# Optimization experiments

Measured on AMD Instinct MI355X. Metric: run time of the kernel, lower is better.

## Reference

```python
import jax, jax.numpy as jnp
import numpy as np
import math

D_MODEL = 1024
D_HIDDEN = 64
H = 16
B = 2
N = 2048


def softmax_one(x, axis=-1):
    # exp(x - max) / (1 + sum(exp(x - max))) -- matches the torch code exactly
    m = jnp.max(x, axis=axis, keepdims=True)
    e = jnp.exp(x - m)
    return e / (1.0 + jnp.sum(e, axis=axis, keepdims=True))


def setup_inputs() -> dict:
    key = jax.random.key(0)
    ks = jax.random.split(key, 8)
    queries = jax.random.normal(ks[0], (B, N, D_MODEL), dtype=jnp.float32)
    keys = jax.random.normal(ks[1], (B, N, D_MODEL), dtype=jnp.float32)
    values = jax.random.normal(ks[2], (B, N, D_MODEL), dtype=jnp.float32)
    std = 0.02
    Wq = std * jax.random.normal(ks[3], (H * D_HIDDEN, D_MODEL), dtype=jnp.float32)
    Wk = std * jax.random.normal(ks[4], (H * D_HIDDEN, D_MODEL), dtype=jnp.float32)
    Wv = std * jax.random.normal(ks[5], (H * D_HIDDEN, D_MODEL), dtype=jnp.float32)
    Wo = std * jax.random.normal(ks[6], (D_MODEL, H * D_HIDDEN), dtype=jnp.float32)
    bq = jnp.zeros((H * D_HIDDEN,), jnp.float32)
    bk = jnp.zeros((H * D_HIDDEN,), jnp.float32)
    bv = jnp.zeros((H * D_HIDDEN,), jnp.float32)
    bo = jnp.zeros((D_MODEL,), jnp.float32)
    return {"queries": queries, "keys": keys, "values": values,
            "Wq": Wq, "bq": bq, "Wk": Wk, "bk": bk,
            "Wv": Wv, "bv": bv, "Wo": Wo, "bo": bo}


def reference(queries, keys, values, Wq, bq, Wk, bk, Wv, bv, Wo, bo):
    b_s, nq, _ = queries.shape
    nk = keys.shape[1]
    # projections: (b, n, h*dh) -> (b, h, n, dh)
    q = (queries @ Wq.T + bq).reshape(b_s, nq, H, D_HIDDEN).transpose(0, 2, 1, 3)
    k = (keys @ Wk.T + bk).reshape(b_s, nk, H, D_HIDDEN).transpose(0, 2, 1, 3)
    v = (values @ Wv.T + bv).reshape(b_s, nk, H, D_HIDDEN).transpose(0, 2, 1, 3)
    scale = 1.0 / math.sqrt(D_HIDDEN)
    scores = jnp.einsum('bhqd,bhkd->bhqk', q, k) * scale  # (b, h, nq, nk)
    attn = softmax_one(scores, axis=-1)  # dropout disabled (eval)
    out = jnp.einsum('bhqk,bhkd->bhqd', attn, v)  # (b, h, nq, dh)
    out = out.transpose(0, 2, 1, 3).reshape(b_s, nq, H * D_HIDDEN)
    out = out @ Wo.T + bo
    present = jnp.stack((k, v))  # (2, b, h, nk, dh)
    return (out, present)
```

## Files before the change

kernel.cpp:

```cpp
#include <hip/hip_runtime.h>
#include <math.h>

#define D_MODEL 1024
#define DH 64
#define NH 16
#define BS 2
#define SEQ 2048
#define MTOT (BS*SEQ)

typedef _Float16 f16x8 __attribute__((ext_vector_type(8)));
typedef _Float16 f16x4 __attribute__((ext_vector_type(4)));
typedef float f32x4 __attribute__((ext_vector_type(4)));

__global__ __launch_bounds__(256) void convert3_kernel(
    const float* __restrict__ s0, const float* __restrict__ s1, const float* __restrict__ s2,
    _Float16* __restrict__ d0, _Float16* __restrict__ d1, _Float16* __restrict__ d2, int n)
{
    const float* s = (blockIdx.y == 0) ? s0 : (blockIdx.y == 1) ? s1 : s2;
    _Float16* d    = (blockIdx.y == 0) ? d0 : (blockIdx.y == 1) ? d1 : d2;
    int i = (blockIdx.x * 256 + threadIdx.x) * 8;
    if (i < n) {
        float4 a = *(const float4*)(s + i);
        float4 b = *(const float4*)(s + i + 4);
        f16x8 o;
        o[0] = (_Float16)a.x; o[1] = (_Float16)a.y; o[2] = (_Float16)a.z; o[3] = (_Float16)a.w;
        o[4] = (_Float16)b.x; o[5] = (_Float16)b.y; o[6] = (_Float16)b.z; o[7] = (_Float16)b.w;
        *(f16x8*)(d + i) = o;
    }
}

__global__ __launch_bounds__(256) void qkv_proj_kernel(
    const _Float16* __restrict__ Xq, const _Float16* __restrict__ Xk, const _Float16* __restrict__ Xv,
    const _Float16* __restrict__ Wq, const _Float16* __restrict__ Wk, const _Float16* __restrict__ Wv,
    const float* __restrict__ bq, const float* __restrict__ bk, const float* __restrict__ bv,
    _Float16* __restrict__ qh, _Float16* __restrict__ kh, _Float16* __restrict__ vt,
    float* __restrict__ outp)
{
    __shared__ __align__(16) _Float16 ldsA[128][40];
    __shared__ __align__(16) _Float16 ldsB[128][40];

    const int jb = blockIdx.x >> 5;
    const int ib = blockIdx.x & 31;
    const int id = jb >> 3;
    const int col0 = (jb & 7) << 7;
    const int row0 = ib << 7;

    const _Float16* X  = (id == 0) ? Xq : (id == 1) ? Xk : Xv;
    const _Float16* W  = (id == 0) ? Wq : (id == 1) ? Wk : Wv;
    const float* bias  = (id == 0) ? bq : (id == 1) ? bk : bv;

    const int tid = threadIdx.x;
    const int w = tid >> 6, lane = tid & 63;
    const int quad = lane >> 4, l16 = lane & 15;
    const int wm = (w >> 1) << 6, wn = (w & 1) << 6;

    const f32x4 zero = {0.f, 0.f, 0.f, 0.f};
    f32x4 acc[4][4];
#pragma unroll
    for (int i = 0; i < 4; i++)
#pragma unroll
        for (int j = 0; j < 4; j++) acc[i][j] = zero;

    for (int k0 = 0; k0 < D_MODEL; k0 += 32) {
        __syncthreads();
#pragma unroll
        for (int i = 0; i < 2; i++) {
            int c = tid + 256 * i;
            int r = c >> 2, c8 = (c & 3) << 3;
            *(f16x8*)&ldsA[r][c8] = *(const f16x8*)(X + (size_t)(row0 + r) * D_MODEL + k0 + c8);
            *(f16x8*)&ldsB[r][c8] = *(const f16x8*)(W + (size_t)(col0 + r) * D_MODEL + k0 + c8);
        }
        __syncthreads();
        f16x8 af[4], bfr[4];
#pragma unroll
        for (int mi = 0; mi < 4; mi++) af[mi]  = *(const f16x8*)&ldsA[wm + mi*16 + l16][quad*8];
#pragma unroll
        for (int ni = 0; ni < 4; ni++) bfr[ni] = *(const f16x8*)&ldsB[wn + ni*16 + l16][quad*8];
#pragma unroll
        for (int mi = 0; mi < 4; mi++)
#pragma unroll
            for (int ni = 0; ni < 4; ni++)
                acc[mi][ni] = __builtin_amdgcn_mfma_f32_16x16x32_f16(af[mi], bfr[ni], acc[mi][ni], 0, 0, 0);
    }

    const size_t OUT0 = (size_t)MTOT * D_MODEL;
    const size_t PRES = (size_t)BS * NH * SEQ * DH;
#pragma unroll
    for (int ni = 0; ni < 4; ni++) {
        int gn = col0 + wn + ni * 16 + l16;
        float bias_v = bias[gn];
        int h = gn >> 6, d = gn & 63;
#pragma unroll
        for (int mi = 0; mi < 4; mi++) {
#pragma unroll
            for (int r = 0; r < 4; r++) {
                int gm = row0 + wm + mi * 16 + quad * 4 + r;
                float val = acc[mi][ni][r] + bias_v;
                int b = gm >> 11, n = gm & 2047;
                size_t bh = (size_t)(b * NH + h);
                size_t idx = (bh * SEQ + n) * DH + d;
                if (id == 0) {
                    qh[idx] = (_Float16)val;
                } else if (id == 1) {
                    outp[OUT0 + idx] = val;
                    kh[idx] = (_Float16)val;
                } else {
                    outp[OUT0 + PRES + idx] = val;
                    vt[(bh * DH + d) * SEQ + n] = (_Float16)val;
                }
            }
        }
    }
}

__global__ __launch_bounds__(256) void attn_kernel(
    const _Float16* __restrict__ qh, const _Float16* __restrict__ kh,
    const _Float16* __restrict__ vt, _Float16* __restrict__ aout)
{
    __shared__ __align__(16) _Float16 Kt[64][72];
    __shared__ __align__(16) _Float16 Vt[64][72];

    const int bh = blockIdx.x & 31;
    const int qt = blockIdx.x >> 5;
    const int b = bh >> 4, h = bh & 15;
    const int tid = threadIdx.x;
    const int w = tid >> 6, lane = tid & 63;
    const int quad = lane >> 4, l16 = lane & 15;
    const int qr0 = qt * 64 + w * 16;

    const _Float16* Qb = qh + (size_t)bh * SEQ * DH;
    const _Float16* Kb = kh + (size_t)bh * SEQ * DH;
    const _Float16* Vb = vt + (size_t)bh * DH * SEQ;

    const float QSCALE = 0.125f * 1.44269504f;
    f16x8 aq[2];
#pragma unroll
    for (int ks = 0; ks < 2; ks++) {
        f16x8 t = *(const f16x8*)(Qb + (size_t)(qr0 + l16) * DH + ks * 32 + quad * 8);
#pragma unroll
        for (int j = 0; j < 8; j++) t[j] = (_Float16)((float)t[j] * QSCALE);
        aq[ks] = t;
    }

    float m2 = -INFINITY, lsum = 0.f;
    const f32x4 zero = {0.f, 0.f, 0.f, 0.f};
    f32x4 accO[4];
#pragma unroll
    for (int db = 0; db < 4; db++) accO[db] = zero;

    for (int kc = 0; kc < SEQ; kc += 64) {
        __syncthreads();
#pragma unroll
        for (int i = 0; i < 2; i++) {
            int c = tid + 256 * i;
            int r = c >> 3, c8 = (c & 7) << 3;
            *(f16x8*)&Kt[r][c8] = *(const f16x8*)(Kb + (size_t)(kc + r) * DH + c8);
            *(f16x8*)&Vt[r][c8] = *(const f16x8*)(Vb + (size_t)r * SEQ + kc + c8);
        }
        __syncthreads();

        f32x4 sT[4];
#pragma unroll
        for (int nb = 0; nb < 4; nb++) sT[nb] = zero;
#pragma unroll
        for (int ks = 0; ks < 2; ks++)
#pragma unroll
            for (int nb = 0; nb < 4; nb++) {
                f16x8 kf = *(const f16x8*)&Kt[nb*16 + l16][ks*32 + quad*8];
                sT[nb] = __builtin_amdgcn_mfma_f32_16x16x32_f16(kf, aq[ks], sT[nb], 0, 0, 0);
            }

        float smax = -INFINITY;
#pragma unroll
        for (int nb = 0; nb < 4; nb++)
#pragma unroll
            for (int r = 0; r < 4; r++) smax = fmaxf(smax, sT[nb][r]);
        smax = fmaxf(smax, __shfl_xor(smax, 16));
        smax = fmaxf(smax, __shfl_xor(smax, 32));
        float m2new = fmaxf(m2, smax);
        float alpha = __builtin_amdgcn_exp2f(m2 - m2new);

        float tsum = 0.f;
#pragma unroll
        for (int nb = 0; nb < 4; nb++)
#pragma unroll
            for (int r = 0; r < 4; r++) {
                float e = __builtin_amdgcn_exp2f(sT[nb][r] - m2new);
                sT[nb][r] = e;
                tsum += e;
            }
        tsum += __shfl_xor(tsum, 16);
        tsum += __shfl_xor(tsum, 32);
        lsum = lsum * alpha + tsum;
        m2 = m2new;

#pragma unroll
        for (int db = 0; db < 4; db++)
#pragma unroll
            for (int r = 0; r < 4; r++) accO[db][r] *= alpha;

        f16x4 pf[4];
#pragma unroll
        for (int nb = 0; nb < 4; nb++)
#pragma unroll
            for (int r = 0; r < 4; r++) pf[nb][r] = (_Float16)sT[nb][r];

#pragma unroll
        for (int db = 0; db < 4; db++)
#pragma unroll
            for (int nb = 0; nb < 4; nb++) {
                f16x4 vf = *(const f16x4*)&Vt[db*16 + l16][nb*16 + quad*4];
                accO[db] = __builtin_amdgcn_mfma_f32_16x16x16f16(vf, pf[nb], accO[db], 0, 0, 0);
            }
    }

    const float inv = 1.f / (1.f + lsum);
    const int q = qr0 + l16;
    _Float16* orow = aout + ((size_t)b * SEQ + q) * D_MODEL + h * DH + quad * 4;
#pragma unroll
    for (int db = 0; db < 4; db++) {
        f16x4 o;
#pragma unroll
        for (int r = 0; r < 4; r++) o[r] = (_Float16)(accO[db][r] * inv);
        *(f16x4*)(orow + db * 16) = o;
    }
}

__global__ __launch_bounds__(256) void out_proj_kernel(
    const _Float16* __restrict__ aout, const _Float16* __restrict__ Wo,
    const float* __restrict__ bo, float* __restrict__ outp)
{
    __shared__ __align__(16) _Float16 ldsA[128][40];
    __shared__ __align__(16) _Float16 ldsB[128][40];

    const int jb = blockIdx.x >> 5;
    const int ib = blockIdx.x & 31;
    const int col0 = jb << 7, row0 = ib << 7;
    const int tid = threadIdx.x;
    const int w = tid >> 6, lane = tid & 63;
    const int quad = lane >> 4, l16 = lane & 15;
    const int wm = (w >> 1) << 6, wn = (w & 1) << 6;

    const f32x4 zero = {0.f, 0.f, 0.f, 0.f};
    f32x4 acc[4][4];
#pragma unroll
    for (int i = 0; i < 4; i++)
#pragma unroll
        for (int j = 0; j < 4; j++) acc[i][j] = zero;

    for (int k0 = 0; k0 < D_MODEL; k0 += 32) {
        __syncthreads();
#pragma unroll
        for (int i = 0; i < 2; i++) {
            int c = tid + 256 * i;
            int r = c >> 2, c8 = (c & 3) << 3;
            *(f16x8*)&ldsA[r][c8] = *(const f16x8*)(aout + (size_t)(row0 + r) * D_MODEL + k0 + c8);
            *(f16x8*)&ldsB[r][c8] = *(const f16x8*)(Wo   + (size_t)(col0 + r) * D_MODEL + k0 + c8);
        }
        __syncthreads();
        f16x8 af[4], bfr[4];
#pragma unroll
        for (int mi = 0; mi < 4; mi++) af[mi]  = *(const f16x8*)&ldsA[wm + mi*16 + l16][quad*8];
#pragma unroll
        for (int ni = 0; ni < 4; ni++) bfr[ni] = *(const f16x8*)&ldsB[wn + ni*16 + l16][quad*8];
#pragma unroll
        for (int mi = 0; mi < 4; mi++)
#pragma unroll
            for (int ni = 0; ni < 4; ni++)
                acc[mi][ni] = __builtin_amdgcn_mfma_f32_16x16x32_f16(af[mi], bfr[ni], acc[mi][ni], 0, 0, 0);
    }

#pragma unroll
    for (int ni = 0; ni < 4; ni++) {
        int gn = col0 + wn + ni * 16 + l16;
        float bias_v = bo[gn];
#pragma unroll
        for (int mi = 0; mi < 4; mi++)
#pragma unroll
            for (int r = 0; r < 4; r++) {
                int gm = row0 + wm + mi * 16 + quad * 4 + r;
                outp[(size_t)gm * D_MODEL + gn] = acc[mi][ni][r] + bias_v;
            }
    }
}

extern "C" void kernel_launch(void* const* d_in, const int* in_sizes, int n_in,
                              void* d_out, int out_size, void* d_ws, size_t ws_size,
                              hipStream_t stream)
{
    const float* queries = (const float*)d_in[0];
    const float* keys    = (const float*)d_in[1];
    const float* values  = (const float*)d_in[2];
    const float* Wq = (const float*)d_in[3];
    const float* bq = (const float*)d_in[4];
    const float* Wk = (const float*)d_in[5];
    const float* bk = (const float*)d_in[6];
    const float* Wv = (const float*)d_in[7];
    const float* bv = (const float*)d_in[8];
    const float* Wo = (const float*)d_in[9];
    const float* bo = (const float*)d_in[10];
    float* outp = (float*)d_out;

    const size_t NELT = (size_t)BS * NH * SEQ * DH;
    const size_t XN   = (size_t)MTOT * D_MODEL;
    const size_t WN   = (size_t)D_MODEL * D_MODEL;
    _Float16* qh   = (_Float16*)d_ws;
    _Float16* kh   = qh + NELT;
    _Float16* vt   = kh + NELT;
    _Float16* aout = vt + NELT;
    _Float16* Xfq  = aout + NELT;
    _Float16* Xfk  = Xfq + XN;
    _Float16* Xfv  = Xfk + XN;
    _Float16* Wfq  = Xfv + XN;
    _Float16* Wfk  = Wfq + WN;
    _Float16* Wfv  = Wfk + WN;
    _Float16* Wfo  = Wfv + WN;

    convert3_kernel<<<dim3((int)(XN/2048), 3), dim3(256), 0, stream>>>(
        queries, keys, values, Xfq, Xfk, Xfv, (int)XN);
    convert3_kernel<<<dim3((int)(WN/2048), 3), dim3(256), 0, stream>>>(
        Wq, Wk, Wv, Wfq, Wfk, Wfv, (int)WN);
    convert3_kernel<<<dim3((int)(WN/2048), 1), dim3(256), 0, stream>>>(
        Wo, Wo, Wo, Wfo, Wfo, Wfo, (int)WN);

    qkv_proj_kernel<<<dim3(768), dim3(256), 0, stream>>>(
        Xfq, Xfk, Xfv, Wfq, Wfk, Wfv, bq, bk, bv, qh, kh, vt, outp);
    attn_kernel<<<dim3(1024), dim3(256), 0, stream>>>(qh, kh, vt, aout);
    out_proj_kernel<<<dim3(256), dim3(256), 0, stream>>>(aout, Wfo, bo, outp);
}
```

Baseline: 278.9 us.

## Merge convert launches, use direct global-to-LDS loads, double-buffer attention K/V

```diff
diff --git a/kernel.cpp b/kernel.cpp
--- a/kernel.cpp
+++ b/kernel.cpp
@@ -11,13 +11,33 @@
 typedef _Float16 f16x8 __attribute__((ext_vector_type(8)));
 typedef _Float16 f16x4 __attribute__((ext_vector_type(4)));
 typedef float f32x4 __attribute__((ext_vector_type(4)));
-
-__global__ __launch_bounds__(256) void convert3_kernel(
+typedef unsigned int u32;
+
+__device__ __forceinline__ void load_lds16(const void* g, void* l) {
+    __builtin_amdgcn_global_load_lds(
+        (const __attribute__((address_space(1))) u32*)g,
+        (__attribute__((address_space(3))) u32*)l, 16, 0, 0);
+}
+
+__global__ __launch_bounds__(256) void convert_all_kernel(
     const float* __restrict__ s0, const float* __restrict__ s1, const float* __restrict__ s2,
-    _Float16* __restrict__ d0, _Float16* __restrict__ d1, _Float16* __restrict__ d2, int n)
-{
-    const float* s = (blockIdx.y == 0) ? s0 : (blockIdx.y == 1) ? s1 : s2;
-    _Float16* d    = (blockIdx.y == 0) ? d0 : (blockIdx.y == 1) ? d1 : d2;
+    const float* __restrict__ s3, const float* __restrict__ s4, const float* __restrict__ s5,
+    const float* __restrict__ s6,
+    _Float16* __restrict__ d0, _Float16* __restrict__ d1, _Float16* __restrict__ d2,
+    _Float16* __restrict__ d3, _Float16* __restrict__ d4, _Float16* __restrict__ d5,
+    _Float16* __restrict__ d6, int nX, int nW)
+{
+    int y = blockIdx.y;
+    const float* s; _Float16* d; int n;
+    switch (y) {
+        case 0: s = s0; d = d0; n = nX; break;
+        case 1: s = s1; d = d1; n = nX; break;
+        case 2: s = s2; d = d2; n = nX; break;
+        case 3: s = s3; d = d3; n = nW; break;
+        case 4: s = s4; d = d4; n = nW; break;
+        case 5: s = s5; d = d5; n = nW; break;
+        default: s = s6; d = d6; n = nW; break;
+    }
     int i = (blockIdx.x * 256 + threadIdx.x) * 8;
     if (i < n) {
         float4 a = *(const float4*)(s + i);
@@ -36,8 +56,8 @@
     _Float16* __restrict__ qh, _Float16* __restrict__ kh, _Float16* __restrict__ vt,
     float* __restrict__ outp)
 {
-    __shared__ __align__(16) _Float16 ldsA[128][40];
-    __shared__ __align__(16) _Float16 ldsB[128][40];
+    __shared__ __align__(16) _Float16 ldsA[128][32];
+    __shared__ __align__(16) _Float16 ldsB[128][32];
 
     const int jb = blockIdx.x >> 5;
     const int ib = blockIdx.x & 31;
@@ -54,6 +74,9 @@
     const int quad = lane >> 4, l16 = lane & 15;
     const int wm = (w >> 1) << 6, wn = (w & 1) << 6;
 
+    const int srow = w * 16 + (lane >> 2);
+    const int scol = (lane & 3) << 3;
+
     const f32x4 zero = {0.f, 0.f, 0.f, 0.f};
     f32x4 acc[4][4];
 #pragma unroll
@@ -65,10 +88,9 @@
         __syncthreads();
 #pragma unroll
         for (int i = 0; i < 2; i++) {
-            int c = tid + 256 * i;
-            int r = c >> 2, c8 = (c & 3) << 3;
-            *(f16x8*)&ldsA[r][c8] = *(const f16x8*)(X + (size_t)(row0 + r) * D_MODEL + k0 + c8);
-            *(f16x8*)&ldsB[r][c8] = *(const f16x8*)(W + (size_t)(col0 + r) * D_MODEL + k0 + c8);
+            int r = i * 64 + srow;
+            load_lds16(X + (size_t)(row0 + r) * D_MODEL + k0 + scol, &ldsA[i * 64 + w * 16][0]);
+            load_lds16(W + (size_t)(col0 + r) * D_MODEL + k0 + scol, &ldsB[i * 64 + w * 16][0]);
         }
         __syncthreads();
         f16x8 af[4], bfr[4];
@@ -117,8 +139,8 @@
     const _Float16* __restrict__ qh, const _Float16* __restrict__ kh,
     const _Float16* __restrict__ vt, _Float16* __restrict__ aout)
 {
-    __shared__ __align__(16) _Float16 Kt[64][72];
-    __shared__ __align__(16) _Float16 Vt[64][72];
+    __shared__ __align__(16) _Float16 Kt[2][64][76];
+    __shared__ __align__(16) _Float16 Vt[2][64][76];
 
     const int bh = blockIdx.x & 31;
     const int qt = blockIdx.x >> 5;
@@ -142,22 +164,36 @@
         aq[ks] = t;
     }
 
+    const int sr0 = tid >> 3, sc = (tid & 7) << 3;
+    const int sr1 = sr0 + 32;
+
+    {
+        *(f16x8*)&Kt[0][sr0][sc] = *(const f16x8*)(Kb + (size_t)sr0 * DH + sc);
+        *(f16x8*)&Kt[0][sr1][sc] = *(const f16x8*)(Kb + (size_t)sr1 * DH + sc);
+        *(f16x8*)&Vt[0][sr0][sc] = *(const f16x8*)(Vb + (size_t)sr0 * SEQ + sc);
+        *(f16x8*)&Vt[0][sr1][sc] = *(const f16x8*)(Vb + (size_t)sr1 * SEQ + sc);
+    }
+    __syncthreads();
+
     float m2 = -INFINITY, lsum = 0.f;
     const f32x4 zero = {0.f, 0.f, 0.f, 0.f};
     f32x4 accO[4];
 #pragma unroll
     for (int db = 0; db < 4; db++) accO[db] = zero;
 
-    for (int kc = 0; kc < SEQ; kc += 64) {
-        __syncthreads();
-#pragma unroll
-        for (int i = 0; i < 2; i++) {
-            int c = tid + 256 * i;
-            int r = c >> 3, c8 = (c & 7) << 3;
-            *(f16x8*)&Kt[r][c8] = *(const f16x8*)(Kb + (size_t)(kc + r) * DH + c8);
-            *(f16x8*)&Vt[r][c8] = *(const f16x8*)(Vb + (size_t)r * SEQ + kc + c8);
-        }
-        __syncthreads();
+    for (int t = 0; t < SEQ / 64; t++) {
+        const int cur = t & 1;
+        const int kc = t * 64;
+
+        f16x8 kr0, kr1, vr0, vr1;
+        if (t + 1 < SEQ / 64) {
+            const _Float16* kp = Kb + (size_t)(kc + 64) * DH;
+            const _Float16* vp = Vb + kc + 64;
+            kr0 = *(const f16x8*)(kp + (size_t)sr0 * DH + sc);
+            kr1 = *(const f16x8*)(kp + (size_t)sr1 * DH + sc);
+            vr0 = *(const f16x8*)(vp + (size_t)sr0 * SEQ + sc);
+            vr1 = *(const f16x8*)(vp + (size_t)sr1 * SEQ + sc);
+        }
 
         f32x4 sT[4];
 #pragma unroll
@@ -166,7 +202,7 @@
         for (int ks = 0; ks < 2; ks++)
 #pragma unroll
             for (int nb = 0; nb < 4; nb++) {
-                f16x8 kf = *(const f16x8*)&Kt[nb*16 + l16][ks*32 + quad*8];
+                f16x8 kf = *(const f16x8*)&Kt[cur][nb*16 + l16][ks*32 + quad*8];
                 sT[nb] = __builtin_amdgcn_mfma_f32_16x16x32_f16(kf, aq[ks], sT[nb], 0, 0, 0);
             }
 
@@ -209,9 +245,17 @@
         for (int db = 0; db < 4; db++)
 #pragma unroll
             for (int nb = 0; nb < 4; nb++) {
-                f16x4 vf = *(const f16x4*)&Vt[db*16 + l16][nb*16 + quad*4];
+                f16x4 vf = *(const f16x4*)&Vt[cur][db*16 + l16][nb*16 + quad*4];
                 accO[db] = __builtin_amdgcn_mfma_f32_16x16x16f16(vf, pf[nb], accO[db], 0, 0, 0);
             }
+
+        if (t + 1 < SEQ / 64) {
+            *(f16x8*)&Kt[cur ^ 1][sr0][sc] = kr0;
+            *(f16x8*)&Kt[cur ^ 1][sr1][sc] = kr1;
+            *(f16x8*)&Vt[cur ^ 1][sr0][sc] = vr0;
+            *(f16x8*)&Vt[cur ^ 1][sr1][sc] = vr1;
+        }
+        __syncthreads();
     }
 
     const float inv = 1.f / (1.f + lsum);
@@ -230,8 +274,8 @@
     const _Float16* __restrict__ aout, const _Float16* __restrict__ Wo,
     const float* __restrict__ bo, float* __restrict__ outp)
 {
-    __shared__ __align__(16) _Float16 ldsA[128][40];
-    __shared__ __align__(16) _Float16 ldsB[128][40];
+    __shared__ __align__(16) _Float16 ldsA[128][32];
+    __shared__ __align__(16) _Float16 ldsB[128][32];
 
     const int jb = blockIdx.x >> 5;
     const int ib = blockIdx.x & 31;
@@ -241,6 +285,9 @@
     const int quad = lane >> 4, l16 = lane & 15;
     const int wm = (w >> 1) << 6, wn = (w & 1) << 6;
 
+    const int srow = w * 16 + (lane >> 2);
+    const int scol = (lane & 3) << 3;
+
     const f32x4 zero = {0.f, 0.f, 0.f, 0.f};
     f32x4 acc[4][4];
 #pragma unroll
@@ -252,10 +299,9 @@
         __syncthreads();
 #pragma unroll
         for (int i = 0; i < 2; i++) {
-            int c = tid + 256 * i;
-            int r = c >> 2, c8 = (c & 3) << 3;
-            *(f16x8*)&ldsA[r][c8] = *(const f16x8*)(aout + (size_t)(row0 + r) * D_MODEL + k0 + c8);
-            *(f16x8*)&ldsB[r][c8] = *(const f16x8*)(Wo   + (size_t)(col0 + r) * D_MODEL + k0 + c8);
+            int r = i * 64 + srow;
+            load_lds16(aout + (size_t)(row0 + r) * D_MODEL + k0 + scol, &ldsA[i * 64 + w * 16][0]);
+            load_lds16(Wo   + (size_t)(col0 + r) * D_MODEL + k0 + scol, &ldsB[i * 64 + w * 16][0]);
         }
         __syncthreads();
         f16x8 af[4], bfr[4];
@@ -316,12 +362,9 @@
     _Float16* Wfv  = Wfk + WN;
     _Float16* Wfo  = Wfv + WN;
 
-    convert3_kernel<<<dim3((int)(XN/2048), 3), dim3(256), 0, stream>>>(
-        queries, keys, values, Xfq, Xfk, Xfv, (int)XN);
-    convert3_kernel<<<dim3((int)(WN/2048), 3), dim3(256), 0, stream>>>(
-        Wq, Wk, Wv, Wfq, Wfk, Wfv, (int)WN);
-    convert3_kernel<<<dim3((int)(WN/2048), 1), dim3(256), 0, stream>>>(
-        Wo, Wo, Wo, Wfo, Wfo, Wfo, (int)WN);
+    convert_all_kernel<<<dim3((int)(XN/2048), 7), dim3(256), 0, stream>>>(
+        queries, keys, values, Wq, Wk, Wv, Wo,
+        Xfq, Xfk, Xfv, Wfq, Wfk, Wfv, Wfo, (int)XN, (int)WN);
 
     qkv_proj_kernel<<<dim3(768), dim3(256), 0, stream>>>(
         Xfq, Xfk, Xfv, Wfq, Wfk, Wfv, bq, bk, bv, qh, kh, vt, outp);
```

After: 265.3 us. -4.9%, faster.
